# Kernel optimization log

Measured on AMD Instinct MI355X. Metric: run time of the kernel, lower is better.

## Reference

```python
import jax, jax.numpy as jnp
import numpy as np

B, C, TX, TY = 32, 384, 512, 2048
NL, K = 2, 3
EPS = 1e-5


def _ln(x, g, b):
    # channel-wise LayerNorm over dim 1 of [B, C, T]
    m = jnp.mean(x, axis=1, keepdims=True)
    v = jnp.mean((x - m) ** 2, axis=1, keepdims=True)
    return (x - m) * jax.lax.rsqrt(v + EPS) * g[None, :, None] + b[None, :, None]


def _conv(x, w, b):
    # x: [B, C, T], w: [O, I, K] -> 'SAME' padding == kernel_size // 2 for odd K
    y = jax.lax.conv_general_dilated(x, w, (1,), 'SAME',
                                     dimension_numbers=('NCH', 'OIH', 'NCH'))
    return y + b[None, :, None]


def _variance_predictor(x, mask, lng, lnb, cw, cb, ow, ob):
    # NL x (LayerNorm -> Conv1d -> SiLU -> [dropout=identity in eval]) * mask
    for i in range(NL):
        h = _conv(_ln(x, lng[i], lnb[i]), cw[i], cb[i])
        x = jax.nn.silu(h) * mask
    return _conv(x, ow, ob) * mask  # [B, 1, T]


def setup_inputs() -> dict:
    key = jax.random.key(0)
    it = iter(jax.random.split(key, 16))
    s = 0.02
    d = {}
    d['x'] = jax.random.normal(next(it), (B, C, TX), jnp.float32)
    d['x_mask'] = jnp.ones((B, 1, TX), jnp.float32)
    d['y_mask'] = jnp.ones((B, 1, TY), jnp.float32)
    d['pitch'] = jax.random.normal(next(it), (B, C, TY), jnp.float32)
    d['energy'] = jax.random.normal(next(it), (B, C, TY), jnp.float32)
    d['path'] = jax.random.uniform(next(it), (B, TX, TY), jnp.float32)
    for p in ('dur', 'pit', 'ene'):
        d[p + '_lng'] = jnp.ones((NL, C), jnp.float32)
        d[p + '_lnb'] = jnp.zeros((NL, C), jnp.float32)
        d[p + '_cw'] = jax.random.normal(next(it), (NL, C, C, K), jnp.float32) * s
        d[p + '_cb'] = jnp.zeros((NL, C), jnp.float32)
        d[p + '_ow'] = jax.random.normal(next(it), (1, C, 1), jnp.float32) * s
        d[p + '_ob'] = jnp.zeros((1,), jnp.float32)
    return d


def reference(x, x_mask, y_mask, pitch, energy, path,
              dur_lng, dur_lnb, dur_cw, dur_cb, dur_ow, dur_ob,
              pit_lng, pit_lnb, pit_cw, pit_cb, pit_ow, pit_ob,
              ene_lng, ene_lnb, ene_cw, ene_cb, ene_ow, ene_ob):
    dur_pred = _variance_predictor(x, x_mask, dur_lng, dur_lnb, dur_cw, dur_cb, dur_ow, dur_ob)
    # LengthRegulator: bmm against duration path matrix [B, TX, TY]
    xe = jnp.einsum('bct,bty->bcy', x, path)  # [B, C, TY]
    pitch_pred = _variance_predictor(xe, y_mask, pit_lng, pit_lnb, pit_cw, pit_cb, pit_ow, pit_ob)
    energy_pred = _variance_predictor(xe, y_mask, ene_lng, ene_lnb, ene_cw, ene_cb, ene_ow, ene_ob)
    out = xe + pitch + energy
    return (out, dur_pred, pitch_pred, energy_pred)
```

## Files before the change

### kernel.cpp

```cpp
#include <hip/hip_runtime.h>

#define B_ 32
#define C_ 384
#define TX_ 512
#define TY_ 2048
#define EPS_ 1e-5f
#define LAY_ ((size_t)(36 * 1536 * 8))

typedef __attribute__((ext_vector_type(8))) short short8;
typedef __attribute__((ext_vector_type(4))) float f32x4;

#define MFMA(a, b, c) __builtin_amdgcn_mfma_f32_16x16x32_bf16(a, b, c, 0, 0, 0)

#define WAITV(N) do { asm volatile("s_waitcnt vmcnt(" #N ")"); \
                      __builtin_amdgcn_sched_barrier(0); } while (0)
#define WAITLK(N) do { asm volatile("s_waitcnt lgkmcnt(" #N ")"); \
                       __builtin_amdgcn_sched_barrier(0); } while (0)
#define SB() __builtin_amdgcn_sched_barrier(0)

typedef unsigned int u32;
__device__ __forceinline__ void gl_lds16(const void* g, void* l) {
    __builtin_amdgcn_global_load_lds(
        (const __attribute__((address_space(1))) u32*)g,
        (__attribute__((address_space(3))) u32*)l, 16, 0, 0);
}

__device__ inline unsigned short f2bf(float f) {
    union { float f; unsigned int u; } v; v.f = f;
    unsigned int r = v.u + 0x7fffu + ((v.u >> 16) & 1u);
    return (unsigned short)(r >> 16);
}
__device__ inline float bf2f(unsigned short s) {
    union { float f; unsigned int u; } v; v.u = ((unsigned int)s) << 16;
    return v.f;
}

template<bool INBF>
__device__ inline float ldx(const void* p, size_t i) {
    if constexpr (INBF) return bf2f(((const unsigned short*)p)[i]);
    else return ((const float*)p)[i];
}

__global__ __launch_bounds__(256) void pack_w2(const float* cw0, const float* cw1,
                                               const float* cw2, const float* g0,
                                               const float* g1, const float* g2,
                                               unsigned short* wp) {
    int idx = blockIdx.x * 256 + threadIdx.x;
    const int NG = 6 * 36 * 384 * 4;
    if (idx >= NG) return;
    int lg = idx & 3;
    int o = (idx >> 2) % 384;
    int c = ((idx >> 2) / 384) % 36;
    int lay = (idx >> 2) / (384 * 36);
    int k = c / 12, ib = c % 12;
    int pr = lay >> 1, l = lay & 1;
    const float* cw = ((pr == 0) ? cw0 : (pr == 1) ? cw1 : cw2) + (size_t)l * C_ * C_ * 3;
    const float* g  = ((pr == 0) ? g0  : (pr == 1) ? g1  : g2)  + (size_t)l * C_;
    const int i0 = ib * 32 + lg * 8;
    short8 v;
    #pragma unroll
    for (int e = 0; e < 8; e++)
        v[e] = (short)f2bf(cw[((size_t)o * C_ + i0 + e) * 3 + k] * g[i0 + e]);
    *(short8*)&wp[(size_t)idx * 8] = v;
}

__global__ __launch_bounds__(256) void bias_fold(
    const float* cw0, const float* cw1, const float* cw2,
    const float* be0, const float* be1, const float* be2,
    const float* cb0, const float* cb1, const float* cb2,
    float* biasT, float* bc0, float* bc2) {
    int idx = blockIdx.x * 256 + threadIdx.x;
    if (idx >= 6 * 384) return;
    int o = idx % 384, lay = idx / 384;
    int pr = lay >> 1, l = lay & 1;
    const float* cw = ((pr == 0) ? cw0 : (pr == 1) ? cw1 : cw2)
                      + (size_t)l * C_ * C_ * 3 + (size_t)o * C_ * 3;
    const float* be = ((pr == 0) ? be0 : (pr == 1) ? be1 : be2) + (size_t)l * C_;
    const float* cb = ((pr == 0) ? cb0 : (pr == 1) ? cb1 : cb2) + (size_t)l * C_;
    float s0 = 0.f, s1 = 0.f, s2 = 0.f;
    for (int i = 0; i < C_; i++) {
        const float b = be[i];
        s0 += cw[i * 3 + 0] * b; s1 += cw[i * 3 + 1] * b; s2 += cw[i * 3 + 2] * b;
    }
    biasT[idx] = cb[o] + s0 + s1 + s2;
    bc0[idx] = s0; bc2[idx] = s2;
}

__global__ __launch_bounds__(256) void pack_x2(const float* x, unsigned short* xp) {
    int idx = blockIdx.x * 256 + threadIdx.x;
    const int NG = B_ * 16 * 384 * 4;
    if (idx >= NG) return;
    int lg = idx & 3;
    int c = (idx >> 2) % 384;
    int q = ((idx >> 2) / 384) % 16;
    int b = (idx >> 2) / (384 * 16);
    const float* src = x + ((size_t)b * C_ + c) * TX_ + q * 32 + lg * 8;
    short8 v;
    #pragma unroll
    for (int e = 0; e < 8; e++) v[e] = (short)f2bf(src[e]);
    *(short8*)&xp[(size_t)idx * 8] = v;
}

__global__ __launch_bounds__(256) void ln_stats_f32(const float* x, float2* st, int T) {
    __shared__ float r1[4][64], r2[4][64];
    int b = blockIdx.y, t0 = blockIdx.x * 64;
    int tl = threadIdx.x & 63, g = threadIdx.x >> 6;
    int t = t0 + tl;
    const float* p = x + (size_t)b * C_ * T + t;
    float s = 0.f, ss = 0.f;
    for (int c = g; c < C_; c += 4) { float v = p[(size_t)c * T]; s += v; ss += v * v; }
    r1[g][tl] = s; r2[g][tl] = ss;
    __syncthreads();
    if (threadIdx.x < 64) {
        float s1 = r1[0][tl] + r1[1][tl] + r1[2][tl] + r1[3][tl];
        float s2 = r2[0][tl] + r2[1][tl] + r2[2][tl] + r2[3][tl];
        float m = s1 * (1.f / C_);
        float var = s2 * (1.f / C_) - m * m;
        st[(size_t)b * T + t0 + tl] = make_float2(m, rsqrtf(var + EPS_));
    }
}

template<bool INBF>
__global__ __launch_bounds__(512, 2) void fused_vp(
    const void* __restrict__ Xin, const float2* __restrict__ stin,
    const unsigned short* __restrict__ W2lay,
    const float* __restrict__ bT,
    const float* __restrict__ c0v, const float* __restrict__ c2v,
    const float* __restrict__ mask,
    float* __restrict__ pred, const float* __restrict__ ow,
    const float* __restrict__ obias, int T)
{
    __shared__ __align__(16) unsigned short xs[132 * 384];
    __shared__ __align__(16) unsigned short wlds[8][2][1536];
    __shared__ float red[260];
    __shared__ float2 st2[130];

    const int tid = threadIdx.x;
    const int b = blockIdx.y;
    const int t0 = blockIdx.x * 128;
    const int lane = tid & 63;
    const int wave = tid >> 6;
    const int lr = lane & 15, lg = lane >> 4;
    const int wm = wave * 48;

    const unsigned short* gbw = W2lay + (size_t)((wm + lr) * 4 + lg) * 8;
    const unsigned short* gbw2 = gbw + LAY_;
    auto STAGE = [&](const unsigned short* base, int c, int buf) {
        #pragma unroll
        for (int fm = 0; fm < 3; fm++)
            gl_lds16(base + (size_t)c * 12288 + fm * 512, &wlds[wave][buf][fm * 512]);
    };
    STAGE(gbw, 0, 0);
    STAGE(gbw, 1, 1);

    {
        const int tl = tid & 127;
        const int tt = 2 + tl;
        const int t = t0 + tl;
        const float2 mr = stin[(size_t)b * T + t];
        const int cg0 = (tid >> 7) * 12;
        for (int i = 0; i < 12; i++) {
            const int cg = cg0 + i;
            const size_t base = ((size_t)b * C_ + cg * 8) * T + t;
            short8 v8;
            #pragma unroll
            for (int j = 0; j < 8; j++)
                v8[j] = (short)f2bf((ldx<INBF>(Xin, base + (size_t)j * T) - mr.x) * mr.y);
            const int ph = (cg & ~7) | ((cg ^ tt) & 7);
            *(short8*)&xs[tt * 384 + ph * 8] = v8;
        }
        if (tid < 192) {
            const int q = tid / 48;
            const int tt2 = (q < 2) ? q : 128 + q;
            const int cg = tid % 48;
            const int t2 = t0 - 2 + tt2;
            short8 v8;
            if (t2 >= 0 && t2 < T) {
                const float2 mr2 = stin[(size_t)b * T + t2];
                const size_t base = ((size_t)b * C_ + cg * 8) * T + t2;
                #pragma unroll
                for (int j = 0; j < 8; j++)
                    v8[j] = (short)f2bf((ldx<INBF>(Xin, base + (size_t)j * T) - mr2.x) * mr2.y);
            } else {
                #pragma unroll
                for (int j = 0; j < 8; j++) v8[j] = 0;
            }
            const int ph = (cg & ~7) | ((cg ^ tt2) & 7);
            *(short8*)&xs[tt2 * 384 + ph * 8] = v8;
        }
    }
    __syncthreads();

    f32x4 acc[3][9];
    const f32x4 zero = {0.f, 0.f, 0.f, 0.f};
    #pragma unroll
    for (int fm = 0; fm < 3; fm++)
        #pragma unroll
        for (int fn = 0; fn < 9; fn++) acc[fm][fn] = zero;

    for (int c = 0; c < 36; ++c) {
        WAITV(3);
        short8 af[3], bf[9];
        #pragma unroll
        for (int fm = 0; fm < 3; fm++)
            af[fm] = *(const short8*)&wlds[wave][c & 1][fm * 512 + lane * 8];
        SB();
        const int k = c / 12, ib = c - k * 12;
        const int cgi = ib * 4 + lg;
        #pragma unroll
        for (int fn = 0; fn < 8; fn++) {
            const int row = 1 + fn * 16 + lr + k;
            const int ph = (cgi & ~7) | ((cgi ^ row) & 7);
            bf[fn] = *(const short8*)&xs[row * 384 + ph * 8];
        }
        {
            const int row = (lr == 1) ? (129 + k) : k;
            const int ph = (cgi & ~7) | ((cgi ^ row) & 7);
            bf[8] = *(const short8*)&xs[row * 384 + ph * 8];
        }
        WAITLK(9);
        if (c < 34) STAGE(gbw, c + 2, c & 1);
        else        STAGE(gbw2, c - 34, c & 1);
        SB();
        __builtin_amdgcn_s_setprio(1);
        #pragma unroll
        for (int fm = 0; fm < 3; fm++)
            #pragma unroll
            for (int fn = 0; fn < 9; fn++)
                acc[fm][fn] = MFMA(af[fm], bf[fn], acc[fm][fn]);
        __builtin_amdgcn_s_setprio(0);
    }

    __syncthreads();
    if (tid < 260) red[tid] = 0.f;
    __syncthreads();

    #pragma unroll
    for (int fn = 0; fn < 8; fn++) {
        const int tt_h = 1 + fn * 16 + lr;
        const int t = t0 + fn * 16 + lr;
        const float mk = mask[(size_t)b * T + t];
        float s1 = 0.f, s2 = 0.f;
        #pragma unroll
        for (int fm = 0; fm < 3; fm++) {
            const int o0 = wm + fm * 16 + lg * 4;
            #pragma unroll
            for (int j = 0; j < 4; j++) {
                float h = acc[fm][fn][j] + bT[o0 + j];
                if (t == 0) h -= c0v[o0 + j];
                if (t == T - 1) h -= c2v[o0 + j];
                const float y = h * (1.f / (1.f + __expf(-h))) * mk;
                acc[fm][fn][j] = y;
                s1 += y; s2 += y * y;
            }
        }
        atomicAdd(&red[tt_h * 2], s1);
        atomicAdd(&red[tt_h * 2 + 1], s2);
    }
    {
        const int tt_h = (lr == 1) ? 129 : 0;
        const int t = t0 - 1 + tt_h;
        const bool inr = (lr < 2) && (t >= 0) && (t < T);
        const float mk = inr ? mask[(size_t)b * T + t] : 0.f;
        float s1 = 0.f, s2 = 0.f;
        #pragma unroll
        for (int fm = 0; fm < 3; fm++) {
            const int o0 = wm + fm * 16 + lg * 4;
            #pragma unroll
            for (int j = 0; j < 4; j++) {
                const float h = acc[fm][8][j] + bT[o0 + j];
                const float y = inr ? (h * (1.f / (1.f + __expf(-h))) * mk) : 0.f;
                acc[fm][8][j] = y;
                s1 += y; s2 += y * y;
            }
        }
        if (inr) {
            atomicAdd(&red[tt_h * 2], s1);
            atomicAdd(&red[tt_h * 2 + 1], s2);
        }
    }
    __syncthreads();

    if (tid < 130) {
        const float s1 = red[tid * 2], s2 = red[tid * 2 + 1];
        const float m = s1 * (1.f / C_);
        const float var = s2 * (1.f / C_) - m * m;
        st2[tid] = make_float2(m, rsqrtf(var + EPS_));
    }
    __syncthreads();

    #pragma unroll
    for (int fn = 0; fn < 8; fn++) {
        const int tt_h = 1 + fn * 16 + lr;
        const float2 mr = st2[tt_h];
        #pragma unroll
        for (int fm = 0; fm < 3; fm++) {
            ushort4 pk;
            #pragma unroll
            for (int j = 0; j < 4; j++)
                ((unsigned short*)&pk)[j] = f2bf((acc[fm][fn][j] - mr.x) * mr.y);
            const int cg = ((wm + fm * 16) >> 3) + (lg >> 1);
            const int ph = (cg & ~7) | ((cg ^ tt_h) & 7);
            *(ushort4*)&xs[tt_h * 384 + ph * 8 + (lg & 1) * 4] = pk;
        }
    }
    if (lr < 2) {
        const int tt_h = (lr == 1) ? 129 : 0;
        const float2 mr = st2[tt_h];
        #pragma unroll
        for (int fm = 0; fm < 3; fm++) {
            ushort4 pk;
            #pragma unroll
            for (int j = 0; j < 4; j++)
                ((unsigned short*)&pk)[j] = f2bf((acc[fm][8][j] - mr.x) * mr.y);
            const int cg = ((wm + fm * 16) >> 3) + (lg >> 1);
            const int ph = (cg & ~7) | ((cg ^ tt_h) & 7);
            *(ushort4*)&xs[tt_h * 384 + ph * 8 + (lg & 1) * 4] = pk;
        }
    }
    __syncthreads();

    f32x4 acc2[3][8];
    #pragma unroll
    for (int fm = 0; fm < 3; fm++)
        #pragma unroll
        for (int fn = 0; fn < 8; fn++) acc2[fm][fn] = zero;

    for (int c = 0; c < 36; ++c) {
        WAITV(3);
        short8 af[3], bf[8];
        #pragma unroll
        for (int fm = 0; fm < 3; fm++)
            af[fm] = *(const short8*)&wlds[wave][c & 1][fm * 512 + lane * 8];
        SB();
        const int k = c / 12, ib = c - k * 12;
        const int cgi = ib * 4 + lg;
        #pragma unroll
        for (int fn = 0; fn < 8; fn++) {
            const int row = fn * 16 + lr + k;
            const int ph = (cgi & ~7) | ((cgi ^ row) & 7);
            bf[fn] = *(const short8*)&xs[row * 384 + ph * 8];
        }
        WAITLK(8);
        STAGE(gbw2, (c + 2 < 36) ? c + 2 : 35, c & 1);
        SB();
        __builtin_amdgcn_s_setprio(1);
        #pragma unroll
        for (int fm = 0; fm < 3; fm++)
            #pragma unroll
            for (int fn = 0; fn < 8; fn++)
                acc2[fm][fn] = MFMA(af[fm], bf[fn], acc2[fm][fn]);
        __builtin_amdgcn_s_setprio(0);
    }

    __syncthreads();
    if (tid < 128) red[tid] = 0.f;
    __syncthreads();
    #pragma unroll
    for (int fn = 0; fn < 8; fn++) {
        const int tl = fn * 16 + lr;
        const int t = t0 + tl;
        const float mk = mask[(size_t)b * T + t];
        float s1 = 0.f;
        #pragma unroll
        for (int fm = 0; fm < 3; fm++) {
            const int o0 = wm + fm * 16 + lg * 4;
            #pragma unroll
            for (int j = 0; j < 4; j++) {
                float h = acc2[fm][fn][j] + bT[384 + o0 + j];
                if (t == 0) h -= c0v[384 + o0 + j];
                if (t == T - 1) h -= c2v[384 + o0 + j];
                const float y = h * (1.f / (1.f + __expf(-h))) * mk;
                s1 += y * ow[o0 + j];
            }
        }
        atomicAdd(&red[tl], s1);
    }
    __syncthreads();
    if (tid < 128) {
        const int t = t0 + tid;
        pred[(size_t)b * T + t] = (red[tid] + obias[0]) * mask[(size_t)b * T + t];
    }
}

__global__ __launch_bounds__(512, 2) void bmm_ln(
    const unsigned short* __restrict__ x2, const float* __restrict__ path,
    const float* __restrict__ pitch, const float* __restrict__ energy,
    float* __restrict__ out, unsigned short* __restrict__ xebf,
    float2* __restrict__ stout, int fused)
{
    __shared__ __align__(16) char smem[81920];
    unsigned short* ps = (unsigned short*)smem;
    typedef unsigned short wbuf_t[2][1536];
    wbuf_t* wlds = (wbuf_t*)(smem + 32768);
    float* red = (float*)(smem + 49152);

    const int tid = threadIdx.x;
    const int bid = blockIdx.x;
    const int work = (bid & 7) * 64 + (bid >> 3);
    const int b = work >> 4;
    const int y0 = (work & 15) << 7;
    const int lane = tid & 63;
    const int wave = tid >> 6;
    const int lr = lane & 15, lg = lane >> 4;
    const int wm = wave * 48;

    const unsigned short* gbx = x2 + ((size_t)b * 16 * 1536 + (size_t)((wm + lr) * 4 + lg)) * 8;
    auto STAGEW = [&](int u, int buf) {
        #pragma unroll
        for (int fm = 0; fm < 3; fm++)
            gl_lds16(gbx + (size_t)u * 12288 + fm * 512, &wlds[wave][buf][fm * 512]);
    };
    STAGEW(0, 0);
    STAGEW(1, 1);

    auto STAGEP = [&](int s) {
        const int yy = tid & 127;
        const int tg = tid >> 7;
        const float* pb = path + ((size_t)b * TX_ + s * 128 + tg * 32) * TY_ + y0 + yy;
        #pragma unroll
        for (int g = 0; g < 4; g++) {
            float vv[8];
            #pragma unroll
            for (int j = 0; j < 8; j++) vv[j] = pb[(size_t)(g * 8 + j) * TY_];
            short8 v8;
            #pragma unroll
            for (int j = 0; j < 8; j++) v8[j] = (short)f2bf(vv[j]);
            const int cg = tg * 4 + g;
            const int ph = (cg & ~7) | ((cg ^ yy) & 7);
            *(short8*)&ps[yy * 128 + ph * 8] = v8;
        }
    };

    f32x4 acc[3][8];
    const f32x4 zero = {0.f, 0.f, 0.f, 0.f};
    #pragma unroll
    for (int fm = 0; fm < 3; fm++)
        #pragma unroll
        for (int fn = 0; fn < 8; fn++) acc[fm][fn] = zero;

    for (int s = 0; s < 4; ++s) {
        if (s) __syncthreads();
        STAGEP(s);
        __syncthreads();
        for (int uu = 0; uu < 4; ++uu) {
            const int u = s * 4 + uu;
            WAITV(3);
            short8 af[3], bf[8];
            #pragma unroll
            for (int fm = 0; fm < 3; fm++)
                af[fm] = *(const short8*)&wlds[wave][u & 1][fm * 512 + lane * 8];
            SB();
            const int cgi = uu * 4 + lg;
            #pragma unroll
            for (int fn = 0; fn < 8; fn++) {
                const int row = fn * 16 + lr;
                const int ph = (cgi & ~7) | ((cgi ^ row) & 7);
                bf[fn] = *(const short8*)&ps[row * 128 + ph * 8];
            }
            WAITLK(8);
            STAGEW((u + 2 < 16) ? u + 2 : 15, u & 1);
            SB();
            __builtin_amdgcn_s_setprio(1);
            #pragma unroll
            for (int fm = 0; fm < 3; fm++)
                #pragma unroll
                for (int fn = 0; fn < 8; fn++)
                    acc[fm][fn] = MFMA(af[fm], bf[fn], acc[fm][fn]);
            __builtin_amdgcn_s_setprio(0);
        }
    }
    WAITV(0);

    __syncthreads();
    if (tid < 256) red[tid] = 0.f;
    __syncthreads();
    #pragma unroll
    for (int fn = 0; fn < 8; fn++) {
        const int yl = fn * 16 + lr;
        float s1 = 0.f, s2 = 0.f;
        #pragma unroll
        for (int fm = 0; fm < 3; fm++)
            #pragma unroll
            for (int j = 0; j < 4; j++) {
                const float v = acc[fm][fn][j];
                s1 += v; s2 += v * v;
            }
        atomicAdd(&red[yl * 2], s1);
        atomicAdd(&red[yl * 2 + 1], s2);
    }

    float* psf = (float*)smem;
    for (int r = 0; r < 4; ++r) {
        __syncthreads();
        if ((wave >> 1) == r) {
            const int cbase = (wave & 1) * 48;
            #pragma unroll
            for (int fn = 0; fn < 8; fn++) {
                const int yl = fn * 16 + lr;
                #pragma unroll
                for (int fm = 0; fm < 3; fm++) {
                    const int cl = cbase + fm * 16 + lg * 4;
                    #pragma unroll
                    for (int j = 0; j < 4; j++)
                        psf[(cl + j) * 128 + yl] = acc[fm][fn][j];
                }
            }
        }
        __syncthreads();
        for (int idx = tid; idx < 96 * 32; idx += 512) {
            const int cl = idx >> 5;
            const int y4 = idx & 31;
            const int c = 96 * r + cl;
            const size_t gi = ((size_t)b * C_ + c) * TY_ + y0 + y4 * 4;
            float4 v = ((float4*)&psf[cl * 128])[y4];
            if (fused) {
                const float4 p = *(const float4*)&pitch[gi];
                const float4 e = *(const float4*)&energy[gi];
                float4 o;
                o.x = v.x + p.x + e.x; o.y = v.y + p.y + e.y;
                o.z = v.z + p.z + e.z; o.w = v.w + p.w + e.w;
                *(float4*)&out[gi] = o;
                ushort4 xb;
                xb.x = f2bf(v.x); xb.y = f2bf(v.y); xb.z = f2bf(v.z); xb.w = f2bf(v.w);
                *(ushort4*)&xebf[gi] = xb;
            } else {
                *(float4*)&out[gi] = v;
            }
        }
    }
    __syncthreads();
    if (tid < 128) {
        const int y = y0 + tid;
        const float s1 = red[tid * 2], s2 = red[tid * 2 + 1];
        const float m = s1 * (1.f / C_);
        const float var = s2 * (1.f / C_) - m * m;
        stout[(size_t)b * TY_ + y] = make_float2(m, rsqrtf(var + EPS_));
    }
}

__global__ __launch_bounds__(256) void add3(float4* o, const float4* p, const float4* e, int n4) {
    for (int i = blockIdx.x * 256 + threadIdx.x; i < n4; i += gridDim.x * 256) {
        float4 a = o[i], x1 = p[i], x2 = e[i];
        a.x += x1.x + x2.x; a.y += x1.y + x2.y;
        a.z += x1.z + x2.z; a.w += x1.w + x2.w;
        o[i] = a;
    }
}

extern "C" void kernel_launch(void* const* d_in, const int* in_sizes, int n_in,
                              void* d_out, int out_size, void* d_ws, size_t ws_size,
                              hipStream_t stream)
{
    const float* x      = (const float*)d_in[0];
    const float* x_mask = (const float*)d_in[1];
    const float* y_mask = (const float*)d_in[2];
    const float* pitch  = (const float*)d_in[3];
    const float* energy = (const float*)d_in[4];
    const float* path   = (const float*)d_in[5];
    const float* prm[3][6];
    for (int p = 0; p < 3; p++)
        for (int q = 0; q < 6; q++)
            prm[p][q] = (const float*)d_in[6 + p * 6 + q];

    float* out         = (float*)d_out;
    float* dur_pred    = out + (size_t)B_ * C_ * TY_;
    float* pitch_pred  = dur_pred + B_ * TX_;
    float* energy_pred = pitch_pred + B_ * TY_;

    const size_t BCTY = (size_t)B_ * C_ * TY_;
    char* w = (char*)d_ws;
    auto alloc = [&](size_t bytes) { char* r = w; w += (bytes + 255) & ~(size_t)255; return r; };

    unsigned short* W2   = (unsigned short*)alloc(6 * LAY_ * 2);
    float* biasT         = (float*)alloc(6 * 384 * 4);
    float* bc0           = (float*)alloc(6 * 384 * 4);
    float* bc2           = (float*)alloc(6 * 384 * 4);
    float2* stA          = (float2*)alloc((size_t)B_ * TY_ * 8);
    unsigned short* x2p  = (unsigned short*)alloc((size_t)B_ * 196608 * 2);
    size_t base_end = (size_t)(w - (char*)d_ws);
    unsigned short* xebf = (unsigned short*)alloc(BCTY * 2);
    size_t xe_end = (size_t)(w - (char*)d_ws);

    const bool haveXe = (xe_end <= ws_size);
    if (base_end > ws_size) return;

    pack_w2<<<dim3((6 * 36 * 384 * 4 + 255) / 256), 256, 0, stream>>>(
        prm[0][2], prm[1][2], prm[2][2], prm[0][0], prm[1][0], prm[2][0], W2);
    bias_fold<<<dim3(9), 256, 0, stream>>>(
        prm[0][2], prm[1][2], prm[2][2], prm[0][1], prm[1][1], prm[2][1],
        prm[0][3], prm[1][3], prm[2][3], biasT, bc0, bc2);
    pack_x2<<<dim3((B_ * 16 * 384 * 4 + 255) / 256), 256, 0, stream>>>(x, x2p);
    ln_stats_f32<<<dim3(TX_ / 64, B_), 256, 0, stream>>>(x, stA, TX_);

    fused_vp<false><<<dim3(TX_ / 128, B_), 512, 0, stream>>>(
        x, stA, W2, biasT, bc0, bc2, x_mask,
        dur_pred, prm[0][4], prm[0][5], TX_);

    bmm_ln<<<dim3(512, 1, 1), 512, 0, stream>>>(
        x2p, path, pitch, energy, out, haveXe ? xebf : nullptr, stA, haveXe ? 1 : 0);

    if (haveXe) {
        fused_vp<true><<<dim3(TY_ / 128, B_), 512, 0, stream>>>(
            xebf, stA, W2 + 2 * LAY_, biasT + 2 * 384, bc0 + 2 * 384, bc2 + 2 * 384,
            y_mask, pitch_pred, prm[1][4], prm[1][5], TY_);
        fused_vp<true><<<dim3(TY_ / 128, B_), 512, 0, stream>>>(
            xebf, stA, W2 + 4 * LAY_, biasT + 4 * 384, bc0 + 4 * 384, bc2 + 4 * 384,
            y_mask, energy_pred, prm[2][4], prm[2][5], TY_);
    } else {
        fused_vp<false><<<dim3(TY_ / 128, B_), 512, 0, stream>>>(
            out, stA, W2 + 2 * LAY_, biasT + 2 * 384, bc0 + 2 * 384, bc2 + 2 * 384,
            y_mask, pitch_pred, prm[1][4], prm[1][5], TY_);
        fused_vp<false><<<dim3(TY_ / 128, B_), 512, 0, stream>>>(
            out, stA, W2 + 4 * LAY_, biasT + 4 * 384, bc0 + 4 * 384, bc2 + 4 * 384,
            y_mask, energy_pred, prm[2][4], prm[2][5], TY_);
        add3<<<dim3(2048), 256, 0, stream>>>((float4*)out, (const float4*)pitch,
                                             (const float4*)energy, B_ * C_ * TY_ / 4);
    }
}
```

Measured before the change: 569.8 us.

## Double-buffer B-fragment LDS reads to overlap with MFMA in conv and bmm loops

Splits the B-operand fragment registers into two buffers (bfA/bfB) and prefetches the next step's LDS fragments before issuing the current step's MFMAs in all three GEMM main loops. This is meant to hide LDS read latency behind matrix-core work instead of stalling on lgkmcnt before each MFMA batch. It raises VGPR pressure (an extra 8–9 short8 fragments per wave), which could lower occupancy or cause spills. The wait counts are still hardcoded and depend on the exact instruction order the compiler emits.

```diff
diff --git a/kernel.cpp b/kernel.cpp
--- a/kernel.cpp
+++ b/kernel.cpp
@@ -198,30 +198,26 @@
         #pragma unroll
         for (int fn = 0; fn < 9; fn++) acc[fm][fn] = zero;
 
-    for (int c = 0; c < 36; ++c) {
-        WAITV(3);
-        short8 af[3], bf[9];
-        #pragma unroll
-        for (int fm = 0; fm < 3; fm++)
-            af[fm] = *(const short8*)&wlds[wave][c & 1][fm * 512 + lane * 8];
-        SB();
+    short8 af[3], bfA[9], bfB[9];
+    auto LOADBF1 = [&](short8* dst, int c) {
         const int k = c / 12, ib = c - k * 12;
         const int cgi = ib * 4 + lg;
         #pragma unroll
         for (int fn = 0; fn < 8; fn++) {
             const int row = 1 + fn * 16 + lr + k;
             const int ph = (cgi & ~7) | ((cgi ^ row) & 7);
-            bf[fn] = *(const short8*)&xs[row * 384 + ph * 8];
-        }
-        {
-            const int row = (lr == 1) ? (129 + k) : k;
-            const int ph = (cgi & ~7) | ((cgi ^ row) & 7);
-            bf[8] = *(const short8*)&xs[row * 384 + ph * 8];
-        }
-        WAITLK(9);
-        if (c < 34) STAGE(gbw, c + 2, c & 1);
-        else        STAGE(gbw2, c - 34, c & 1);
-        SB();
+            dst[fn] = *(const short8*)&xs[row * 384 + ph * 8];
+        }
+        const int rowh = (lr == 1) ? (129 + k) : k;
+        const int phh = (cgi & ~7) | ((cgi ^ rowh) & 7);
+        dst[8] = *(const short8*)&xs[rowh * 384 + phh * 8];
+    };
+    auto LOADAF = [&](int c) {
+        #pragma unroll
+        for (int fm = 0; fm < 3; fm++)
+            af[fm] = *(const short8*)&wlds[wave][c & 1][fm * 512 + lane * 8];
+    };
+    auto FMAS1 = [&](short8* bf) {
         __builtin_amdgcn_s_setprio(1);
         #pragma unroll
         for (int fm = 0; fm < 3; fm++)
@@ -229,6 +225,26 @@
             for (int fn = 0; fn < 9; fn++)
                 acc[fm][fn] = MFMA(af[fm], bf[fn], acc[fm][fn]);
         __builtin_amdgcn_s_setprio(0);
+    };
+    auto STAGE1 = [&](int s) {
+        if (s + 2 < 36) STAGE(gbw, s + 2, s & 1);
+        else            STAGE(gbw2, s - 34, s & 1);
+    };
+
+    LOADBF1(bfA, 0);
+    for (int c = 0; c < 36; c += 2) {
+        WAITV(3);
+        LOADAF(c); SB();
+        LOADBF1(bfB, c + 1);
+        WAITLK(9);
+        STAGE1(c); SB();
+        FMAS1(bfA);
+        WAITV(3);
+        LOADAF(c + 1); SB();
+        LOADBF1(bfA, (c + 2 < 36) ? c + 2 : 35);
+        WAITLK(9);
+        STAGE1(c + 1); SB();
+        FMAS1(bfB);
     }
 
     __syncthreads();
@@ -326,24 +342,17 @@
         #pragma unroll
         for (int fn = 0; fn < 8; fn++) acc2[fm][fn] = zero;
 
-    for (int c = 0; c < 36; ++c) {
-        WAITV(3);
-        short8 af[3], bf[8];
-        #pragma unroll
-        for (int fm = 0; fm < 3; fm++)
-            af[fm] = *(const short8*)&wlds[wave][c & 1][fm * 512 + lane * 8];
-        SB();
+    auto LOADBF2 = [&](short8* dst, int c) {
         const int k = c / 12, ib = c - k * 12;
         const int cgi = ib * 4 + lg;
         #pragma unroll
         for (int fn = 0; fn < 8; fn++) {
             const int row = fn * 16 + lr + k;
             const int ph = (cgi & ~7) | ((cgi ^ row) & 7);
-            bf[fn] = *(const short8*)&xs[row * 384 + ph * 8];
-        }
-        WAITLK(8);
-        STAGE(gbw2, (c + 2 < 36) ? c + 2 : 35, c & 1);
-        SB();
+            dst[fn] = *(const short8*)&xs[row * 384 + ph * 8];
+        }
+    };
+    auto FMAS2 = [&](short8* bf) {
         __builtin_amdgcn_s_setprio(1);
         #pragma unroll
         for (int fm = 0; fm < 3; fm++)
@@ -351,6 +360,25 @@
             for (int fn = 0; fn < 8; fn++)
                 acc2[fm][fn] = MFMA(af[fm], bf[fn], acc2[fm][fn]);
         __builtin_amdgcn_s_setprio(0);
+    };
+    auto STAGE2 = [&](int s) {
+        STAGE(gbw2, (s + 2 < 36) ? s + 2 : 35, s & 1);
+    };
+
+    LOADBF2(bfA, 0);
+    for (int c = 0; c < 36; c += 2) {
+        WAITV(3);
+        LOADAF(c); SB();
+        LOADBF2(bfB, c + 1);
+        WAITLK(8);
+        STAGE2(c); SB();
+        FMAS2(bfA);
+        WAITV(3);
+        LOADAF(c + 1); SB();
+        LOADBF2(bfA, (c + 2 < 36) ? c + 2 : 35);
+        WAITLK(8);
+        STAGE2(c + 1); SB();
+        FMAS2(bfB);
     }
 
     __syncthreads();
@@ -439,36 +467,52 @@
         #pragma unroll
         for (int fn = 0; fn < 8; fn++) acc[fm][fn] = zero;
 
+    short8 af[3], bfA[8], bfB[8];
+    auto LOADAF = [&](int u) {
+        #pragma unroll
+        for (int fm = 0; fm < 3; fm++)
+            af[fm] = *(const short8*)&wlds[wave][u & 1][fm * 512 + lane * 8];
+    };
+    auto LOADBF = [&](short8* dst, int uu) {
+        const int cgi = uu * 4 + lg;
+        #pragma unroll
+        for (int fn = 0; fn < 8; fn++) {
+            const int row = fn * 16 + lr;
+            const int ph = (cgi & ~7) | ((cgi ^ row) & 7);
+            dst[fn] = *(const short8*)&ps[row * 128 + ph * 8];
+        }
+    };
+    auto FMAS = [&](short8* bf) {
+        __builtin_amdgcn_s_setprio(1);
+        #pragma unroll
+        for (int fm = 0; fm < 3; fm++)
+            #pragma unroll
+            for (int fn = 0; fn < 8; fn++)
+                acc[fm][fn] = MFMA(af[fm], bf[fn], acc[fm][fn]);
+        __builtin_amdgcn_s_setprio(0);
+    };
+
     for (int s = 0; s < 4; ++s) {
         if (s) __syncthreads();
         STAGEP(s);
         __syncthreads();
-        for (int uu = 0; uu < 4; ++uu) {
-            const int u = s * 4 + uu;
-            WAITV(3);
-            short8 af[3], bf[8];
-            #pragma unroll
-            for (int fm = 0; fm < 3; fm++)
-                af[fm] = *(const short8*)&wlds[wave][u & 1][fm * 512 + lane * 8];
-            SB();
-            const int cgi = uu * 4 + lg;
-            #pragma unroll
-            for (int fn = 0; fn < 8; fn++) {
-                const int row = fn * 16 + lr;
-                const int ph = (cgi & ~7) | ((cgi ^ row) & 7);
-                bf[fn] = *(const short8*)&ps[row * 128 + ph * 8];
-            }
-            WAITLK(8);
-            STAGEW((u + 2 < 16) ? u + 2 : 15, u & 1);
-            SB();
-            __builtin_amdgcn_s_setprio(1);
-            #pragma unroll
-            for (int fm = 0; fm < 3; fm++)
-                #pragma unroll
-                for (int fn = 0; fn < 8; fn++)
-                    acc[fm][fn] = MFMA(af[fm], bf[fn], acc[fm][fn]);
-            __builtin_amdgcn_s_setprio(0);
-        }
+        const int u0 = s * 4;
+        LOADBF(bfA, 0);
+        WAITV(3); LOADAF(u0); SB();
+        LOADBF(bfB, 1);
+        WAITLK(8); STAGEW((u0 + 2 < 16) ? u0 + 2 : 15, u0 & 1); SB();
+        FMAS(bfA);
+        WAITV(3); LOADAF(u0 + 1); SB();
+        LOADBF(bfA, 2);
+        WAITLK(8); STAGEW((u0 + 3 < 16) ? u0 + 3 : 15, (u0 + 1) & 1); SB();
+        FMAS(bfB);
+        WAITV(3); LOADAF(u0 + 2); SB();
+        LOADBF(bfB, 3);
+        WAITLK(8); STAGEW((u0 + 4 < 16) ? u0 + 4 : 15, (u0 + 2) & 1); SB();
+        FMAS(bfA);
+        WAITV(3); LOADAF(u0 + 3); SB();
+        WAITLK(0); STAGEW((u0 + 5 < 16) ? u0 + 5 : 15, (u0 + 3) & 1); SB();
+        FMAS(bfB);
     }
     WAITV(0);
 
```

Result: no change. 577.3 us (+1.3%).
